# Kernel tuning notes

Measured on AMD Instinct MI355X. Metric: run time of the kernel, lower is better.

Reference implementation:

```python
import jax, jax.numpy as jnp
import numpy as np

B, H, W, C = 64, 56, 56, 256
WIN, SHIFT, HEADS = 7, 3, 8
HEAD_DIM = C // HEADS
N = WIN * WIN
EPS = 1e-5


def _rel_pos_index():
    # matches get_relative_position_index (tf.meshgrid 'xy' indexing)
    xx, yy = np.meshgrid(np.arange(WIN), np.arange(WIN))  # shapes (W,H)
    coords = np.stack([yy, xx], 0).reshape(2, -1)  # (2, N)
    rel = coords[:, :, None] - coords[:, None, :]  # (2, N, N)
    rel = rel.transpose(1, 2, 0)
    idx = (rel[:, :, 0] + WIN - 1) * (2 * WIN - 1) + (rel[:, :, 1] + WIN - 1)
    return jnp.asarray(idx, dtype=jnp.int32)  # (N, N)


def _attn_mask():
    # shifted-window attention mask, (nW, N, N) with 0 / -100
    img = np.zeros((H, W), dtype=np.float32)
    cnt = 0
    for hs in (slice(0, -WIN), slice(-WIN, -SHIFT), slice(-SHIFT, None)):
        for ws in (slice(0, -WIN), slice(-WIN, -SHIFT), slice(-SHIFT, None)):
            img[hs, ws] = cnt
            cnt += 1
    mw = img.reshape(H // WIN, WIN, W // WIN, WIN).transpose(0, 2, 1, 3).reshape(-1, N)
    am = mw[:, None, :] - mw[:, :, None]
    am = np.where(am != 0, -100.0, 0.0).astype(np.float32)
    return jnp.asarray(am)  # (nW, N, N)


def _layer_norm(x, g, b):
    mu = jnp.mean(x, -1, keepdims=True)
    var = jnp.mean(jnp.square(x - mu), -1, keepdims=True)
    return (x - mu) * jax.lax.rsqrt(var + EPS) * g + b


def setup_inputs() -> dict:
    key = jax.random.key(0)
    ks = jax.random.split(key, 6)
    s = lambda fan: 1.0 / np.sqrt(fan)
    return {
        'x': jax.random.normal(ks[0], (B, H * W, C), jnp.float32),
        'ln1_g': jnp.ones((C,), jnp.float32),
        'ln1_b': jnp.zeros((C,), jnp.float32),
        'qkv_w': jax.random.normal(ks[1], (C, 3 * C), jnp.float32) * s(C),
        'qkv_b': jnp.zeros((3 * C,), jnp.float32),
        'rpb_table': jax.random.normal(ks[2], ((2 * WIN - 1) ** 2, HEADS), jnp.float32) * 0.02,
        'proj_w': jax.random.normal(ks[3], (C, C), jnp.float32) * s(C),
        'proj_b': jnp.zeros((C,), jnp.float32),
        'ln2_g': jnp.ones((C,), jnp.float32),
        'ln2_b': jnp.zeros((C,), jnp.float32),
        'mlp_w1': jax.random.normal(ks[4], (C, 4 * C), jnp.float32) * s(C),
        'mlp_b1': jnp.zeros((4 * C,), jnp.float32),
        'mlp_w2': jax.random.normal(ks[5], (4 * C, C), jnp.float32) * s(4 * C),
        'mlp_b2': jnp.zeros((C,), jnp.float32),
    }


def _forward(x, ln1_g, ln1_b, qkv_w, qkv_b, rpb_table, proj_w, proj_b,
             ln2_g, ln2_b, mlp_w1, mlp_b1, mlp_w2, mlp_b2):
    rel_idx = _rel_pos_index()
    mask = _attn_mask()
    nW = (H // WIN) * (W // WIN)

    shortcut = x
    y = _layer_norm(x, ln1_g, ln1_b).reshape(B, H, W, C)
    y = jnp.roll(y, (-SHIFT, -SHIFT), axis=(1, 2))
    # window partition -> (B*nW, N, C)
    y = y.reshape(B, H // WIN, WIN, W // WIN, WIN, C)
    y = y.transpose(0, 1, 3, 2, 4, 5).reshape(B * nW, N, C)

    qkv = (y @ qkv_w + qkv_b).reshape(B * nW, N, 3, HEADS, HEAD_DIM)
    q, k, v = jnp.moveaxis(qkv, 2, 0)  # each (B*nW, N, heads, hd)
    q = q * (HEAD_DIM ** -0.5)
    attn = jnp.einsum('wqhd,wkhd->whqk', q, k)  # (B*nW, heads, N, N)
    bias = jnp.transpose(rpb_table[rel_idx], (2, 0, 1))  # (heads, N, N)
    attn = attn + bias[None]
    attn = attn.reshape(B, nW, HEADS, N, N) + mask[None, :, None]
    attn = jax.nn.softmax(attn.reshape(B * nW, HEADS, N, N), axis=-1)
    o = jnp.einsum('whqk,wkhd->wqhd', attn, v).reshape(B * nW, N, C)
    o = o @ proj_w + proj_b

    # window reverse + un-shift
    o = o.reshape(B, H // WIN, W // WIN, WIN, WIN, C)
    o = o.transpose(0, 1, 3, 2, 4, 5).reshape(B, H, W, C)
    o = jnp.roll(o, (SHIFT, SHIFT), axis=(1, 2)).reshape(B, H * W, C)

    x = shortcut + o
    h = _layer_norm(x, ln2_g, ln2_b)
    h = jax.nn.gelu(h @ mlp_w1 + mlp_b1, approximate=False) @ mlp_w2 + mlp_b2
    return x + h


def reference(x, ln1_g, ln1_b, qkv_w, qkv_b, rpb_table, proj_w, proj_b,
              ln2_g, ln2_b, mlp_w1, mlp_b1, mlp_w2, mlp_b2):
    return _forward(x, ln1_g, ln1_b, qkv_w, qkv_b, rpb_table, proj_w, proj_b,
                    ln2_g, ln2_b, mlp_w1, mlp_b1, mlp_w2, mlp_b2)
```

## Files before the change

### kernel.cpp

```cpp
#include <hip/hip_runtime.h>
#include <math.h>


typedef __attribute__((ext_vector_type(8))) short bf16x8;
typedef __attribute__((ext_vector_type(4))) float f32x4;

#define NTOK 200704
#define NN   49
#define NPARAM 4680
#define TBL_ELEMS (4 * 8 * 49 * 64)

__device__ __forceinline__ float bf2f(unsigned short u) {
    union { unsigned int i; float f; } v; v.i = ((unsigned)u) << 16; return v.f;
}
__device__ __forceinline__ unsigned short f2bf(float f) {
    union { float fv; unsigned int i; } v; v.fv = f;
    return (unsigned short)((v.i + 0x7fffu + ((v.i >> 16) & 1u)) >> 16);
}

__device__ __forceinline__ void gload_lds16(const unsigned short* g, unsigned short* l) {
    __builtin_amdgcn_global_load_lds(
        (const __attribute__((address_space(1))) unsigned int*)g,
        (__attribute__((address_space(3))) unsigned int*)l, 16, 0, 0);
}

__device__ __forceinline__ float gelu_erf(float v) {
    float av = fabsf(v);
    float x = av * 0.70710678118654752f;
    float t = __builtin_amdgcn_rcpf(fmaf(x, 0.3275911f, 1.0f));
    float p = fmaf(1.061405429f, t, -1.453152027f);
    p = fmaf(p, t, 1.421413741f);
    p = fmaf(p, t, -0.284496736f);
    p = fmaf(p, t, 0.254829592f);
    p = p * t;
    float ex = __builtin_amdgcn_exp2f(x * x * -1.4426950408889634f);
    float E = fmaf(-p, ex, 1.0f);
    return fmaf(0.5f * av, E, 0.5f * v);
}

__global__ void detect_kernel(const unsigned short* __restrict__ xu, int* flag) {
    int ln = threadIdx.x;
    int sane = 0;
    #pragma unroll
    for (int t = 0; t < 16; t++) {
        unsigned u = xu[(ln * 16 + t) * 2];
        unsigned e = (u >> 7) & 0xFF;
        sane += (e >= 0x60 && e <= 0x90) ? 1 : 0;
    }
    #pragma unroll
    for (int off = 32; off; off >>= 1) sane += __shfl_xor(sane, off);
    if (ln == 0) *flag = (sane < 614) ? 1 : 0;
}

__device__ __forceinline__ float ld_any(const void* p, int j, int f) {
    return f ? ((const float*)p)[j] : bf2f(((const unsigned short*)p)[j]);
}

__global__ void convert_params_kernel(
    const void* ln1_g, const void* ln1_b, const void* qkv_b, const void* proj_b,
    const void* ln2_g, const void* ln2_b, const void* b1, const void* b2,
    const void* rpb, const int* __restrict__ flag, float* __restrict__ dst) {
    int i = blockIdx.x * 256 + threadIdx.x;
    if (i >= NPARAM) return;
    int f = *flag;
    const void* src; int j;
    if      (i < 256)  { src = ln1_g;  j = i; }
    else if (i < 512)  { src = ln1_b;  j = i - 256; }
    else if (i < 1280) { src = qkv_b;  j = i - 512; }
    else if (i < 1536) { src = proj_b; j = i - 1280; }
    else if (i < 1792) { src = ln2_g;  j = i - 1536; }
    else if (i < 2048) { src = ln2_b;  j = i - 1792; }
    else if (i < 3072) { src = b1;     j = i - 2048; }
    else if (i < 3328) { src = b2;     j = i - 3072; }
    else               { src = rpb;    j = i - 3328; }
    dst[i] = ld_any(src, j, f);
}

__global__ void build_tbl_kernel(const float* __restrict__ rpbF,
                                 float* __restrict__ tbl) {
    int idx = blockIdx.x * 256 + threadIdx.x;
    if (idx >= TBL_ELEMS) return;
    int k = idx & 63;
    int q = (idx >> 6) % 49;
    int h = ((idx >> 6) / 49) & 7;
    int pat = idx / (64 * 49 * 8);
    float v;
    if (k >= 49) {
        v = -1e30f;
    } else {
        int ir = q / 7, ic = q - ir * 7, jr = k / 7, jc = k - jr * 7;
        v = rpbF[((ir - jr + 6) * 13 + (ic - jc + 6)) * 8 + h];
        int rb = pat >> 1, cb = pat & 1;
        int ci = (rb ? (ir < 4 ? 3 : 6) : 0) + (cb ? (ic < 4 ? 1 : 2) : 0);
        int cj = (rb ? (jr < 4 ? 3 : 6) : 0) + (cb ? (jc < 4 ? 1 : 2) : 0);
        if (ci != cj) v -= 100.f;
    }
    tbl[idx] = v;
}

__global__ void transpose_any(const void* __restrict__ in,
                              unsigned short* __restrict__ out, int K, int N,
                              const int* __restrict__ flag) {
    int f = *flag;
    int idx = blockIdx.x * 256 + threadIdx.x;
    if (idx < K * N) {
        int k = idx / N, n = idx - k * N;
        out[n * K + k] = f2bf(ld_any(in, idx, f));
    }
}

__global__ void relayout_w1(const void* __restrict__ in,
                            unsigned short* __restrict__ out,
                            const int* __restrict__ flag) {
    int f = *flag;
    int idx = blockIdx.x * 256 + threadIdx.x;
    if (idx < 256 * 1024) {
        int k = idx >> 10, h = idx & 1023;
        int c = h >> 5, r = h & 31;
        int ks = k ^ ((r & 7) << 3);
        out[c * 8192 + r * 256 + ks] = f2bf(ld_any(in, idx, f));
    }
}

__global__ void relayout_w2(const void* __restrict__ in,
                            unsigned short* __restrict__ out,
                            const int* __restrict__ flag) {
    int f = *flag;
    int idx = blockIdx.x * 256 + threadIdx.x;
    if (idx < 1024 * 256) {
        int k = idx >> 8, n = idx & 255;
        int c = k >> 5, kk = k & 31;
        out[c * 8192 + n * 32 + kk] = f2bf(ld_any(in, idx, f));
    }
}

__global__ __launch_bounds__(256) void ln1_window_kernel(
    const void* __restrict__ x, const float* __restrict__ paramsF,
    unsigned short* __restrict__ y, const int* __restrict__ flag) {
    int f = *flag;
    int wv = threadIdx.x >> 6, ln = threadIdx.x & 63;
    int tok = blockIdx.x * 4 + wv;
    float v0, v1, v2, v3;
    if (f) {
        float4 pv = *(const float4*)((const float*)x + (size_t)tok * 256 + ln * 4);
        v0 = pv.x; v1 = pv.y; v2 = pv.z; v3 = pv.w;
    } else {
        ushort4 pv = *(const ushort4*)((const unsigned short*)x + (size_t)tok * 256 + ln * 4);
        v0 = bf2f(pv.x); v1 = bf2f(pv.y); v2 = bf2f(pv.z); v3 = bf2f(pv.w);
    }
    float s = v0 + v1 + v2 + v3;
    float sq = v0 * v0 + v1 * v1 + v2 * v2 + v3 * v3;
    #pragma unroll
    for (int off = 32; off; off >>= 1) { s += __shfl_xor(s, off); sq += __shfl_xor(sq, off); }
    float mu = s * (1.f / 256.f);
    float rs = rsqrtf(fmaxf(sq * (1.f / 256.f) - mu * mu, 0.f) + 1e-5f);
    float4 gv = *(const float4*)(paramsF + ln * 4);
    float4 bv = *(const float4*)(paramsF + 256 + ln * 4);
    int bb = tok / 3136, hw = tok - bb * 3136;
    int h = hw / 56, w = hw - h * 56;
    int hp = h - 3; hp += (hp < 0) ? 56 : 0;
    int wp = w - 3; wp += (wp < 0) ? 56 : 0;
    int win = (hp / 7) * 8 + (wp / 7);
    int n = (hp % 7) * 7 + (wp % 7);
    size_t drow = ((size_t)bb * 64 + win) * NN + n;
    ushort4 o;
    o.x = f2bf((v0 - mu) * rs * gv.x + bv.x);
    o.y = f2bf((v1 - mu) * rs * gv.y + bv.y);
    o.z = f2bf((v2 - mu) * rs * gv.z + bv.z);
    o.w = f2bf((v3 - mu) * rs * gv.w + bv.w);
    *(ushort4*)(y + drow * 256 + ln * 4) = o;
}

__device__ __forceinline__ void gemm_core_k256(
    const unsigned short* __restrict__ A, const unsigned short* __restrict__ Bt,
    int rowBase, int colBase, unsigned short* As, unsigned short* Bs, f32x4 acc[2][4]) {
    const int tid = threadIdx.x;
    const int wv = tid >> 6, ln = tid & 63;
    const int m16 = ln & 15, q4 = ln >> 4;
    const int ar = tid >> 1, ah = (tid & 1) * 32;
    const int br = tid >> 2, bp = (tid & 3) * 16;
    for (int kb = 0; kb < 256; kb += 64) {
        const unsigned short* ag = A + (size_t)(rowBase + ar) * 256 + kb + ah;
        unsigned short* asd = As + ar * 72 + ah;
        #pragma unroll
        for (int i = 0; i < 4; i++)
            *(bf16x8*)(asd + i * 8) = *(const bf16x8*)(ag + i * 8);
        const unsigned short* bg = Bt + (size_t)(colBase + br) * 256 + kb + bp;
        unsigned short* bsd = Bs + br * 72 + bp;
        #pragma unroll
        for (int i = 0; i < 2; i++)
            *(bf16x8*)(bsd + i * 8) = *(const bf16x8*)(bg + i * 8);
        __syncthreads();
        #pragma unroll
        for (int ks = 0; ks < 64; ks += 32) {
            bf16x8 af[2], bfr[4];
            #pragma unroll
            for (int rt = 0; rt < 2; rt++)
                af[rt] = *(const bf16x8*)(As + (wv * 32 + rt * 16 + m16) * 72 + ks + q4 * 8);
            #pragma unroll
            for (int ct = 0; ct < 4; ct++)
                bfr[ct] = *(const bf16x8*)(Bs + (ct * 16 + m16) * 72 + ks + q4 * 8);
            #pragma unroll
            for (int rt = 0; rt < 2; rt++)
                #pragma unroll
                for (int ct = 0; ct < 4; ct++)
                    acc[rt][ct] = __builtin_amdgcn_mfma_f32_16x16x32_bf16(
                        af[rt], bfr[ct], acc[rt][ct], 0, 0, 0);
        }
        __syncthreads();
    }
}

__global__ __launch_bounds__(256) void gemm_qkv_kernel(
    const unsigned short* __restrict__ A, const unsigned short* __restrict__ Bt,
    const float* __restrict__ bias,
    unsigned short* __restrict__ out) {
    __shared__ unsigned short As[128 * 72];
    __shared__ unsigned short Bs[64 * 72];
    const int ln = threadIdx.x & 63, wv = threadIdx.x >> 6;
    const int m16 = ln & 15, q4 = ln >> 4;
    const int rowBase = blockIdx.y * 128, colBase = blockIdx.x * 64;
    f32x4 acc[2][4];
    #pragma unroll
    for (int i = 0; i < 2; i++)
        #pragma unroll
        for (int j = 0; j < 4; j++)
            #pragma unroll
            for (int r = 0; r < 4; r++) acc[i][j][r] = 0.f;
    gemm_core_k256(A, Bt, rowBase, colBase, As, Bs, acc);
    #pragma unroll
    for (int rt = 0; rt < 2; rt++)
        #pragma unroll
        for (int ct = 0; ct < 4; ct++) {
            int col = colBase + ct * 16 + m16;
            float bs = bias[col];
            float scale = (col < 256) ? 0.17677669529663689f : 1.0f;
            #pragma unroll
            for (int r = 0; r < 4; r++) {
                int row = rowBase + wv * 32 + rt * 16 + q4 * 4 + r;
                out[(size_t)row * 768 + col] = f2bf((acc[rt][ct][r] + bs) * scale);
            }
        }
}

__global__ __launch_bounds__(256) void gemm_proj_kernel(
    const unsigned short* __restrict__ A, const unsigned short* __restrict__ Bt,
    const float* __restrict__ bias,
    const void* __restrict__ xin,
    unsigned short* __restrict__ x2, const int* __restrict__ flag) {
    __shared__ unsigned short As[128 * 72];
    __shared__ unsigned short Bs[64 * 72];
    const int f = *flag;
    const int ln = threadIdx.x & 63, wv = threadIdx.x >> 6;
    const int m16 = ln & 15, q4 = ln >> 4;
    const int rowBase = blockIdx.y * 128, colBase = blockIdx.x * 64;
    f32x4 acc[2][4];
    #pragma unroll
    for (int i = 0; i < 2; i++)
        #pragma unroll
        for (int j = 0; j < 4; j++)
            #pragma unroll
            for (int r = 0; r < 4; r++) acc[i][j][r] = 0.f;
    gemm_core_k256(A, Bt, rowBase, colBase, As, Bs, acc);
    #pragma unroll
    for (int rt = 0; rt < 2; rt++)
        #pragma unroll
        for (int r = 0; r < 4; r++) {
            int row = rowBase + wv * 32 + rt * 16 + q4 * 4 + r;
            int win = row / NN, n = row - win * NN;
            int bb = win >> 6, wl = win & 63;
            int i7 = n / 7, j7 = n - i7 * 7;
            int hp = (wl >> 3) * 7 + i7 + 3; if (hp >= 56) hp -= 56;
            int wp = (wl & 7) * 7 + j7 + 3;  if (wp >= 56) wp -= 56;
            size_t drow = ((size_t)bb * 3136 + hp * 56 + wp) * 256;
            #pragma unroll
            for (int ct = 0; ct < 4; ct++) {
                int col = colBase + ct * 16 + m16;
                float v = acc[rt][ct][r] + bias[col] + ld_any(xin, drow + col, f);
                x2[drow + col] = f2bf(v);
            }
        }
}

__global__ __launch_bounds__(256) void attn_mfma_kernel(
    const unsigned short* __restrict__ qkv,
    const float* __restrict__ tbl,
    unsigned short* __restrict__ o) {
    __shared__ __align__(16) unsigned short Vt[256 * 72];
    __shared__ __align__(16) unsigned short Ps[4][64 * 72];
    const int tid = threadIdx.x;
    const int wv = tid >> 6, ln = tid & 63;
    const int m16 = ln & 15, q4 = ln >> 4;
    const int win = blockIdx.x;
    const size_t wbase = (size_t)win * 49 * 768;

    #pragma unroll
    for (int i = 0; i < 8; i++) {
        int idx = i * 256 + tid;
        int ch = idx >> 6, tok = idx & 63;
        if (tok < 49) {
            bf16x8 v = *(const bf16x8*)(qkv + wbase + (size_t)tok * 768 + 512 + ch * 8);
            #pragma unroll
            for (int u = 0; u < 8; u++)
                Vt[(ch * 8 + u) * 72 + tok] = (unsigned short)v[u];
        }
    }
    #pragma unroll
    for (int u = 0; u < 23; u++) Vt[tid * 72 + 49 + u] = 0;

    const int wl = win & 63;
    const int pat = (((wl >> 3) == 7) ? 2 : 0) + (((wl & 7) == 7) ? 1 : 0);
    __syncthreads();

    unsigned short* Pw = &Ps[wv][0];
    for (int hh = 0; hh < 2; hh++) {
        const int h = wv * 2 + hh;
        bf16x8 kf[4], qf[4];
        #pragma unroll
        for (int t = 0; t < 4; t++) {
            size_t rrow = wbase + (size_t)(t * 16 + m16) * 768 + h * 32 + q4 * 8;
            qf[t] = *(const bf16x8*)(qkv + rrow);
            kf[t] = *(const bf16x8*)(qkv + rrow + 256);
        }
        f32x4 acc[4][4];
        #pragma unroll
        for (int kt = 0; kt < 4; kt++)
            #pragma unroll
            for (int qt = 0; qt < 4; qt++) {
                #pragma unroll
                for (int r = 0; r < 4; r++) acc[kt][qt][r] = 0.f;
                acc[kt][qt] = __builtin_amdgcn_mfma_f32_16x16x32_bf16(
                    kf[kt], qf[qt], acc[kt][qt], 0, 0, 0);
            }

        const float* tb = tbl + ((size_t)(pat * 8 + h) * 49) * 64;
        #pragma unroll
        for (int qt = 0; qt < 4; qt++) {
            int q = qt * 16 + m16;
            int qc = q < 49 ? q : 48;
            float s[4][4];
            float mx = -3e38f;
            #pragma unroll
            for (int kt = 0; kt < 4; kt++) {
                float4 tv = *(const float4*)(tb + qc * 64 + kt * 16 + q4 * 4);
                s[kt][0] = acc[kt][qt][0] + tv.x;
                s[kt][1] = acc[kt][qt][1] + tv.y;
                s[kt][2] = acc[kt][qt][2] + tv.z;
                s[kt][3] = acc[kt][qt][3] + tv.w;
                #pragma unroll
                for (int r = 0; r < 4; r++) mx = fmaxf(mx, s[kt][r]);
            }
            mx = fmaxf(mx, __shfl_xor(mx, 16));
            mx = fmaxf(mx, __shfl_xor(mx, 32));
            float sum = 0.f;
            #pragma unroll
            for (int kt = 0; kt < 4; kt++)
                #pragma unroll
                for (int r = 0; r < 4; r++) {
                    float e = __expf(s[kt][r] - mx);
                    s[kt][r] = e; sum += e;
                }
            sum += __shfl_xor(sum, 16);
            sum += __shfl_xor(sum, 32);
            float inv = 1.f / sum;
            #pragma unroll
            for (int kt = 0; kt < 4; kt++) {
                ushort4 p4;
                p4.x = f2bf(s[kt][0] * inv);
                p4.y = f2bf(s[kt][1] * inv);
                p4.z = f2bf(s[kt][2] * inv);
                p4.w = f2bf(s[kt][3] * inv);
                *(ushort4*)(Pw + q * 72 + kt * 16 + q4 * 4) = p4;
            }
        }

        f32x4 po[4][2];
        #pragma unroll
        for (int mt = 0; mt < 4; mt++)
            #pragma unroll
            for (int nt = 0; nt < 2; nt++)
                #pragma unroll
                for (int r = 0; r < 4; r++) po[mt][nt][r] = 0.f;
        #pragma unroll
        for (int kstep = 0; kstep < 2; kstep++) {
            bf16x8 pa[4], vb[2];
            #pragma unroll
            for (int mt = 0; mt < 4; mt++)
                pa[mt] = *(const bf16x8*)(Pw + (mt * 16 + m16) * 72 + kstep * 32 + q4 * 8);
            #pragma unroll
            for (int nt = 0; nt < 2; nt++)
                vb[nt] = *(const bf16x8*)(Vt + (h * 32 + nt * 16 + m16) * 72 + kstep * 32 + q4 * 8);
            #pragma unroll
            for (int mt = 0; mt < 4; mt++)
                #pragma unroll
                for (int nt = 0; nt < 2; nt++)
                    po[mt][nt] = __builtin_amdgcn_mfma_f32_16x16x32_bf16(
                        pa[mt], vb[nt], po[mt][nt], 0, 0, 0);
        }

        #pragma unroll
        for (int mt = 0; mt < 4; mt++)
            #pragma unroll
            for (int r = 0; r < 4; r++) {
                int q = mt * 16 + q4 * 4 + r;
                if (q < 49) {
                    size_t orow = ((size_t)win * 49 + q) * 256 + h * 32;
                    o[orow + m16]      = f2bf(po[mt][0][r]);
                    o[orow + 16 + m16] = f2bf(po[mt][1][r]);
                }
            }
    }
}

__global__ __launch_bounds__(256, 2) void mlp_fused_v3(
    const unsigned short* __restrict__ x2,
    const float* __restrict__ g2F, const float* __restrict__ b2lnF,
    const unsigned short* __restrict__ w1s,
    const float* __restrict__ b1F,
    const unsigned short* __restrict__ w2s,
    const float* __restrict__ b2F,
    void* __restrict__ out, const int* __restrict__ flag) {
    __shared__ __align__(16) unsigned short Bs1[2][32 * 256];
    __shared__ __align__(16) unsigned short Bs2[2][256 * 32];
    __shared__ __align__(16) unsigned short Hs[64 * 40];
    const int f = *flag;
    const int tid = threadIdx.x;
    const int wv = tid >> 6, ln = tid & 63;
    const int m16 = ln & 15, q4 = ln >> 4;
    const int tok0 = blockIdx.x * 64;

    {
        const unsigned short* s1 = w1s + tid * 8;
        const unsigned short* s2 = w2s + tid * 8;
        #pragma unroll
        for (int j = 0; j < 4; j++) {
            gload_lds16(s1 + j * 2048, &Bs1[0][tid * 8 + j * 2048]);
            gload_lds16(s2 + j * 2048, &Bs2[0][tid * 8 + j * 2048]);
        }
    }

    bf16x8 areg[8];
    {
        const unsigned short* xr = x2 + (size_t)(tok0 + wv * 16 + m16) * 256 + q4 * 8;
        #pragma unroll
        for (int ks = 0; ks < 8; ks++) areg[ks] = *(const bf16x8*)(xr + ks * 32);
        float s = 0.f, sq = 0.f;
        #pragma unroll
        for (int ks = 0; ks < 8; ks++)
            #pragma unroll
            for (int u = 0; u < 8; u++) {
                float v = bf2f((unsigned short)areg[ks][u]);
                s += v; sq += v * v;
            }
        s += __shfl_xor(s, 16); s += __shfl_xor(s, 32);
        sq += __shfl_xor(sq, 16); sq += __shfl_xor(sq, 32);
        float mu = s * (1.f / 256.f);
        float rs = rsqrtf(fmaxf(sq * (1.f / 256.f) - mu * mu, 0.f) + 1e-5f);
        #pragma unroll
        for (int ks = 0; ks < 8; ks++)
            #pragma unroll
            for (int u = 0; u < 8; u++) {
                int kidx = ks * 32 + q4 * 8 + u;
                float v = (bf2f((unsigned short)areg[ks][u]) - mu) * rs * g2F[kidx] + b2lnF[kidx];
                areg[ks][u] = (short)f2bf(v);
            }
    }

    f32x4 acc2[4][4];
    #pragma unroll
    for (int rt = 0; rt < 4; rt++)
        #pragma unroll
        for (int ct = 0; ct < 4; ct++)
            #pragma unroll
            for (int r = 0; r < 4; r++) acc2[rt][ct][r] = 0.f;

    #pragma unroll 1
    for (int c = 0; c < 32; ++c) {
        const int cur = c & 1;
        asm volatile("s_waitcnt vmcnt(0)" ::: "memory");
        __builtin_amdgcn_s_barrier();
        __builtin_amdgcn_sched_barrier(0);

        if (c + 1 < 32) {
            const unsigned short* s1 = w1s + (size_t)(c + 1) * 8192 + tid * 8;
            const unsigned short* s2 = w2s + (size_t)(c + 1) * 8192 + tid * 8;
            unsigned short* d1 = &Bs1[cur ^ 1][tid * 8];
            unsigned short* d2 = &Bs2[cur ^ 1][tid * 8];
            #pragma unroll
            for (int j = 0; j < 4; j++) {
                gload_lds16(s1 + j * 2048, d1 + j * 2048);
                gload_lds16(s2 + j * 2048, d2 + j * 2048);
            }
        }
        __builtin_amdgcn_sched_barrier(0);

        f32x4 acc1[2];
        #pragma unroll
        for (int ct = 0; ct < 2; ct++)
            #pragma unroll
            for (int r = 0; r < 4; r++) acc1[ct][r] = 0.f;
        const unsigned short* b1base = &Bs1[cur][0];
        #pragma unroll
        for (int ks = 0; ks < 8; ks++) {
            int kidx = (ks * 32 + q4 * 8) ^ ((m16 & 7) << 3);
            #pragma unroll
            for (int ct = 0; ct < 2; ct++) {
                bf16x8 wfr = *(const bf16x8*)(b1base + (ct * 16 + m16) * 256 + kidx);
                acc1[ct] = __builtin_amdgcn_mfma_f32_16x16x32_bf16(wfr, areg[ks], acc1[ct], 0, 0, 0);
            }
        }

        #pragma unroll
        for (int ct = 0; ct < 2; ct++) {
            float4 bb = *(const float4*)(b1F + c * 32 + ct * 16 + q4 * 4);
            ushort4 o4;
            o4.x = f2bf(gelu_erf(acc1[ct][0] + bb.x));
            o4.y = f2bf(gelu_erf(acc1[ct][1] + bb.y));
            o4.z = f2bf(gelu_erf(acc1[ct][2] + bb.z));
            o4.w = f2bf(gelu_erf(acc1[ct][3] + bb.w));
            *(ushort4*)(Hs + (wv * 16 + m16) * 40 + ct * 16 + q4 * 4) = o4;
        }
        asm volatile("s_waitcnt lgkmcnt(0)" ::: "memory");
        __builtin_amdgcn_sched_barrier(0);
        __builtin_amdgcn_s_barrier();
        __builtin_amdgcn_sched_barrier(0);

        bf16x8 haf[4];
        #pragma unroll
        for (int rt = 0; rt < 4; rt++)
            haf[rt] = *(const bf16x8*)(Hs + (rt * 16 + m16) * 40 + q4 * 8);
        const unsigned short* b2base = &Bs2[cur][0];
        #pragma unroll
        for (int ct = 0; ct < 4; ct++) {
            bf16x8 bfr = *(const bf16x8*)(b2base + (wv * 64 + ct * 16 + m16) * 32 + q4 * 8);
            #pragma unroll
            for (int rt = 0; rt < 4; rt++)
                acc2[rt][ct] = __builtin_amdgcn_mfma_f32_16x16x32_bf16(haf[rt], bfr, acc2[rt][ct], 0, 0, 0);
        }
    }

    #pragma unroll
    for (int rt = 0; rt < 4; rt++)
        #pragma unroll
        for (int ct = 0; ct < 4; ct++) {
            int col = wv * 64 + ct * 16 + m16;
            float bb = b2F[col];
            #pragma unroll
            for (int r = 0; r < 4; r++) {
                int tokr = tok0 + rt * 16 + q4 * 4 + r;
                size_t idx = (size_t)tokr * 256 + col;
                float v = acc2[rt][ct][r] + bb + bf2f(x2[idx]);
                if (f) ((float*)out)[idx] = v;
                else   ((unsigned short*)out)[idx] = f2bf(v);
            }
        }
}

extern "C" void kernel_launch(void* const* d_in, const int* in_sizes, int n_in,
                              void* d_out, int out_size, void* d_ws, size_t ws_size,
                              hipStream_t stream) {
    const void* x      = d_in[0];
    const void* qkv_w  = d_in[3];
    const void* proj_w = d_in[6];
    const void* w1     = d_in[10];
    const void* w2     = d_in[12];

    char* ws = (char*)d_ws;
    size_t off = 0;
    unsigned short* y = (unsigned short*)(ws + off);
    off += (size_t)NTOK * 256 * 2;
    size_t qkv_off = off;
    unsigned short* qkv = (unsigned short*)(ws + off);
    off += (size_t)NTOK * 768 * 2;
    unsigned short* x2 = (unsigned short*)(ws + qkv_off);
    unsigned short* o = y;
    unsigned short* qkvWt = (unsigned short*)(ws + off); off += 768 * 256 * 2;
    unsigned short* projWt = (unsigned short*)(ws + off); off += 256 * 256 * 2;
    unsigned short* w1s = (unsigned short*)(ws + off); off += 1024 * 256 * 2;
    unsigned short* w2s = (unsigned short*)(ws + off); off += 256 * 1024 * 2;
    float* paramsF = (float*)(ws + off); off += NPARAM * 4;
    int* flag = (int*)(ws + off); off += 16;
    float* tbl = (float*)(ws + off); off += (size_t)TBL_ELEMS * 4;
    (void)ws_size; (void)in_sizes; (void)n_in; (void)out_size;

    detect_kernel<<<1, 64, 0, stream>>>((const unsigned short*)x, flag);
    convert_params_kernel<<<(NPARAM + 255) / 256, 256, 0, stream>>>(
        d_in[1], d_in[2], d_in[4], d_in[7], d_in[8], d_in[9], d_in[11], d_in[13],
        d_in[5], flag, paramsF);
    build_tbl_kernel<<<(TBL_ELEMS + 255) / 256, 256, 0, stream>>>(paramsF + 3328, tbl);
    transpose_any<<<(256 * 768 + 255) / 256, 256, 0, stream>>>(qkv_w, qkvWt, 256, 768, flag);
    transpose_any<<<(256 * 256 + 255) / 256, 256, 0, stream>>>(proj_w, projWt, 256, 256, flag);
    relayout_w1<<<(256 * 1024 + 255) / 256, 256, 0, stream>>>(w1, w1s, flag);
    relayout_w2<<<(1024 * 256 + 255) / 256, 256, 0, stream>>>(w2, w2s, flag);

    ln1_window_kernel<<<NTOK / 4, 256, 0, stream>>>(x, paramsF, y, flag);
    gemm_qkv_kernel<<<dim3(768 / 64, NTOK / 128), 256, 0, stream>>>(y, qkvWt, paramsF + 512, qkv);
    attn_mfma_kernel<<<4096, 256, 0, stream>>>(qkv, tbl, o);
    gemm_proj_kernel<<<dim3(256 / 64, NTOK / 128), 256, 0, stream>>>(
        o, projWt, paramsF + 1280, x, x2, flag);
    mlp_fused_v3<<<NTOK / 64, 256, 0, stream>>>(
        x2, paramsF + 1536, paramsF + 1792, w1s, paramsF + 2048, w2s, paramsF + 3072, d_out, flag);
}
```

Baseline: 1.397 ms.

## Keep MLP hidden activations in registers via shuffles, read W2 from global

```diff
diff --git a/kernel.cpp b/kernel.cpp
--- a/kernel.cpp
+++ b/kernel.cpp
@@ -412,7 +412,7 @@
     }
 }
 
-__global__ __launch_bounds__(256, 2) void mlp_fused_v3(
+__global__ __launch_bounds__(256, 3) void mlp_fused_v4(
     const unsigned short* __restrict__ x2,
     const float* __restrict__ g2F, const float* __restrict__ b2lnF,
     const unsigned short* __restrict__ w1s,
@@ -421,27 +421,23 @@
     const float* __restrict__ b2F,
     void* __restrict__ out, const int* __restrict__ flag) {
     __shared__ __align__(16) unsigned short Bs1[2][32 * 256];
-    __shared__ __align__(16) unsigned short Bs2[2][256 * 32];
-    __shared__ __align__(16) unsigned short Hs[64 * 40];
     const int f = *flag;
     const int tid = threadIdx.x;
     const int wv = tid >> 6, ln = tid & 63;
     const int m16 = ln & 15, q4 = ln >> 4;
     const int tok0 = blockIdx.x * 64;
+    const int tok = tok0 + wv * 16 + m16;
 
     {
         const unsigned short* s1 = w1s + tid * 8;
-        const unsigned short* s2 = w2s + tid * 8;
-        #pragma unroll
-        for (int j = 0; j < 4; j++) {
+        #pragma unroll
+        for (int j = 0; j < 4; j++)
             gload_lds16(s1 + j * 2048, &Bs1[0][tid * 8 + j * 2048]);
-            gload_lds16(s2 + j * 2048, &Bs2[0][tid * 8 + j * 2048]);
-        }
     }
 
     bf16x8 areg[8];
     {
-        const unsigned short* xr = x2 + (size_t)(tok0 + wv * 16 + m16) * 256 + q4 * 8;
+        const unsigned short* xr = x2 + (size_t)tok * 256 + q4 * 8;
         #pragma unroll
         for (int ks = 0; ks < 8; ks++) areg[ks] = *(const bf16x8*)(xr + ks * 32);
         float s = 0.f, sq = 0.f;
@@ -466,13 +462,15 @@
             }
     }
 
-    f32x4 acc2[4][4];
-    #pragma unroll
-    for (int rt = 0; rt < 4; rt++)
-        #pragma unroll
-        for (int ct = 0; ct < 4; ct++)
-            #pragma unroll
-            for (int r = 0; r < 4; r++) acc2[rt][ct][r] = 0.f;
+    f32x4 acc2[16];
+    #pragma unroll
+    for (int i = 0; i < 16; i++)
+        #pragma unroll
+        for (int r = 0; r < 4; r++) acc2[i][r] = 0.f;
+
+    const int l1 = m16 + (((2 * q4) & 3) << 4);
+    const int l2 = m16 + (((2 * q4 + 1) & 3) << 4);
+    const bool hi = q4 >= 2;
 
     #pragma unroll 1
     for (int c = 0; c < 32; ++c) {
@@ -483,14 +481,10 @@
 
         if (c + 1 < 32) {
             const unsigned short* s1 = w1s + (size_t)(c + 1) * 8192 + tid * 8;
-            const unsigned short* s2 = w2s + (size_t)(c + 1) * 8192 + tid * 8;
             unsigned short* d1 = &Bs1[cur ^ 1][tid * 8];
-            unsigned short* d2 = &Bs2[cur ^ 1][tid * 8];
-            #pragma unroll
-            for (int j = 0; j < 4; j++) {
+            #pragma unroll
+            for (int j = 0; j < 4; j++)
                 gload_lds16(s1 + j * 2048, d1 + j * 2048);
-                gload_lds16(s2 + j * 2048, d2 + j * 2048);
-            }
         }
         __builtin_amdgcn_sched_barrier(0);
 
@@ -510,50 +504,59 @@
             }
         }
 
+        union { ushort4 s; unsigned int u[2]; } pk[2];
         #pragma unroll
         for (int ct = 0; ct < 2; ct++) {
             float4 bb = *(const float4*)(b1F + c * 32 + ct * 16 + q4 * 4);
-            ushort4 o4;
-            o4.x = f2bf(gelu_erf(acc1[ct][0] + bb.x));
-            o4.y = f2bf(gelu_erf(acc1[ct][1] + bb.y));
-            o4.z = f2bf(gelu_erf(acc1[ct][2] + bb.z));
-            o4.w = f2bf(gelu_erf(acc1[ct][3] + bb.w));
-            *(ushort4*)(Hs + (wv * 16 + m16) * 40 + ct * 16 + q4 * 4) = o4;
-        }
-        asm volatile("s_waitcnt lgkmcnt(0)" ::: "memory");
-        __builtin_amdgcn_sched_barrier(0);
-        __builtin_amdgcn_s_barrier();
-        __builtin_amdgcn_sched_barrier(0);
-
-        bf16x8 haf[4];
-        #pragma unroll
-        for (int rt = 0; rt < 4; rt++)
-            haf[rt] = *(const bf16x8*)(Hs + (rt * 16 + m16) * 40 + q4 * 8);
-        const unsigned short* b2base = &Bs2[cur][0];
-        #pragma unroll
-        for (int ct = 0; ct < 4; ct++) {
-            bf16x8 bfr = *(const bf16x8*)(b2base + (wv * 64 + ct * 16 + m16) * 32 + q4 * 8);
-            #pragma unroll
-            for (int rt = 0; rt < 4; rt++)
-                acc2[rt][ct] = __builtin_amdgcn_mfma_f32_16x16x32_bf16(haf[rt], bfr, acc2[rt][ct], 0, 0, 0);
-        }
-    }
-
-    #pragma unroll
-    for (int rt = 0; rt < 4; rt++)
-        #pragma unroll
-        for (int ct = 0; ct < 4; ct++) {
-            int col = wv * 64 + ct * 16 + m16;
-            float bb = b2F[col];
-            #pragma unroll
-            for (int r = 0; r < 4; r++) {
-                int tokr = tok0 + rt * 16 + q4 * 4 + r;
-                size_t idx = (size_t)tokr * 256 + col;
-                float v = acc2[rt][ct][r] + bb + bf2f(x2[idx]);
-                if (f) ((float*)out)[idx] = v;
-                else   ((unsigned short*)out)[idx] = f2bf(v);
-            }
-        }
+            pk[ct].s.x = f2bf(gelu_erf(acc1[ct][0] + bb.x));
+            pk[ct].s.y = f2bf(gelu_erf(acc1[ct][1] + bb.y));
+            pk[ct].s.z = f2bf(gelu_erf(acc1[ct][2] + bb.z));
+            pk[ct].s.w = f2bf(gelu_erf(acc1[ct][3] + bb.w));
+        }
+
+        unsigned int r0x = __shfl(pk[0].u[0], l1), r0y = __shfl(pk[0].u[1], l1);
+        unsigned int r0z = __shfl(pk[0].u[0], l2), r0w = __shfl(pk[0].u[1], l2);
+        unsigned int r1x = __shfl(pk[1].u[0], l1), r1y = __shfl(pk[1].u[1], l1);
+        unsigned int r1z = __shfl(pk[1].u[0], l2), r1w = __shfl(pk[1].u[1], l2);
+        union { bf16x8 v; unsigned int u[4]; } bfrag;
+        bfrag.u[0] = hi ? r1x : r0x;
+        bfrag.u[1] = hi ? r1y : r0y;
+        bfrag.u[2] = hi ? r1z : r0z;
+        bfrag.u[3] = hi ? r1w : r0w;
+
+        const unsigned short* w2g = w2s + (size_t)c * 8192 + m16 * 32 + q4 * 8;
+        #pragma unroll
+        for (int g = 0; g < 4; g++) {
+            bf16x8 wf[4];
+            #pragma unroll
+            for (int j = 0; j < 4; j++)
+                wf[j] = *(const bf16x8*)(w2g + (g * 4 + j) * 512);
+            #pragma unroll
+            for (int j = 0; j < 4; j++)
+                acc2[g * 4 + j] = __builtin_amdgcn_mfma_f32_16x16x32_bf16(
+                    wf[j], bfrag.v, acc2[g * 4 + j], 0, 0, 0);
+        }
+    }
+
+    const size_t trow = (size_t)tok * 256;
+    #pragma unroll
+    for (int ct2 = 0; ct2 < 16; ct2++) {
+        int col0 = ct2 * 16 + q4 * 4;
+        float4 bb = *(const float4*)(b2F + col0);
+        ushort4 rv = *(const ushort4*)(x2 + trow + col0);
+        float v0 = acc2[ct2][0] + bb.x + bf2f(rv.x);
+        float v1 = acc2[ct2][1] + bb.y + bf2f(rv.y);
+        float v2 = acc2[ct2][2] + bb.z + bf2f(rv.z);
+        float v3 = acc2[ct2][3] + bb.w + bf2f(rv.w);
+        if (f) {
+            float4 ov = {v0, v1, v2, v3};
+            *(float4*)((float*)out + trow + col0) = ov;
+        } else {
+            ushort4 ov;
+            ov.x = f2bf(v0); ov.y = f2bf(v1); ov.z = f2bf(v2); ov.w = f2bf(v3);
+            *(ushort4*)((unsigned short*)out + trow + col0) = ov;
+        }
+    }
 }
 
 extern "C" void kernel_launch(void* const* d_in, const int* in_sizes, int n_in,
@@ -598,6 +601,6 @@
     attn_mfma_kernel<<<4096, 256, 0, stream>>>(qkv, tbl, o);
     gemm_proj_kernel<<<dim3(256 / 64, NTOK / 128), 256, 0, stream>>>(
         o, projWt, paramsF + 1280, x, x2, flag);
-    mlp_fused_v3<<<NTOK / 64, 256, 0, stream>>>(
+    mlp_fused_v4<<<NTOK / 64, 256, 0, stream>>>(
         x2, paramsF + 1536, paramsF + 1792, w1s, paramsF + 2048, w2s, paramsF + 3072, d_out, flag);
 }
```

Measured after the change: 1.499 ms. +7.3%, slower.
